# Kernel optimization log

Measured on AMD Instinct MI355X. Metric: run time of the kernel, lower is better.

Reference implementation:

```python
import jax, jax.numpy as jnp
import numpy as np

N_NODES = 20000  # number of batch nodes (static for segment ops)

def setup_inputs() -> dict:
    key = jax.random.key(0)
    N, E, V, D = N_NODES, 640000, 100000, 64
    ks = jax.random.split(key, 8)
    nodes = jax.random.randint(ks[0], (N,), 0, V)
    neigh_idx = jax.random.randint(ks[1], (E,), 0, V)
    seg_ids = jnp.sort(jax.random.randint(ks[2], (E,), 0, N))  # ragged degrees, sorted by node
    u2e = jax.random.normal(ks[3], (V, D), jnp.float32) * 0.02
    s1 = 1.0 / np.sqrt(2 * D)
    s2 = 1.0 / np.sqrt(D)
    att1_w = jax.random.uniform(ks[4], (2 * D, D), jnp.float32, -s1, s1)
    att1_b = jnp.zeros((D,), jnp.float32)
    att2_w = jax.random.uniform(ks[5], (D, D), jnp.float32, -s2, s2)
    att2_b = jnp.zeros((D,), jnp.float32)
    att3_w = jax.random.uniform(ks[6], (D, 1), jnp.float32, -s2, s2)
    att3_b = jnp.zeros((1,), jnp.float32)
    return dict(nodes=nodes, neigh_idx=neigh_idx, seg_ids=seg_ids, u2e=u2e,
                att1_w=att1_w, att1_b=att1_b, att2_w=att2_w, att2_b=att2_b,
                att3_w=att3_w, att3_b=att3_b)


def reference(nodes, neigh_idx, seg_ids, u2e, att1_w, att1_b, att2_w, att2_b, att3_w, att3_b):
    # Ragged per-node neighbor attention, flattened over all edges.
    e_u = u2e[neigh_idx]              # [E, D] neighbor embeddings
    u_rep = u2e[nodes][seg_ids]       # [E, D] center-node embedding broadcast per edge
    x = jnp.concatenate([e_u, u_rep], axis=1)            # [E, 2D]
    x = jax.nn.relu(x @ att1_w + att1_b)                  # [E, D]
    x = jax.nn.relu(x @ att2_w + att2_b)                  # [E, D]
    logits = (x @ att3_w + att3_b)[:, 0]                  # [E]
    # segment softmax over each node's neighbor set
    m = jax.ops.segment_max(logits, seg_ids, num_segments=N_NODES)
    m = jnp.where(jnp.isfinite(m), m, 0.0)                # guard empty segments
    ex = jnp.exp(logits - m[seg_ids])
    denom = jax.ops.segment_sum(ex, seg_ids, num_segments=N_NODES)
    att = ex / jnp.maximum(denom[seg_ids], 1e-9)          # [E]
    # attention-weighted sum of neighbor embeddings per node (e_u^T @ att_w per node)
    out = jax.ops.segment_sum(att[:, None] * e_u, seg_ids, num_segments=N_NODES)  # [N, D]
    return out
```

## Files before the change

### kernel.cpp

```cpp
#include <hip/hip_runtime.h>
#include <hip/hip_bf16.h>

typedef __attribute__((ext_vector_type(8))) short bf16x8;
typedef __attribute__((ext_vector_type(4))) float f32x4;

__device__ __forceinline__ unsigned short f2bf(float f) {
    unsigned x = __float_as_uint(f);
    unsigned r = (x + 0x7FFF + ((x >> 16) & 1)) >> 16;
    return (unsigned short)r;
}
__device__ __forceinline__ bf16x8 cvt8(const float* __restrict__ p) {
    bf16x8 r;
#pragma unroll
    for (int j = 0; j < 8; ++j) r[j] = (short)f2bf(p[j]);
    return r;
}
__device__ __forceinline__ unsigned pack_relu_bf16(unsigned yv, unsigned zv) {
    float lo = fmaxf(__uint_as_float(yv << 16) + __uint_as_float(zv << 16), 0.0f);
    float hi = fmaxf(__uint_as_float(yv & 0xFFFF0000u) + __uint_as_float(zv & 0xFFFF0000u), 0.0f);
    __hip_bfloat162 p = __float22bfloat162_rn(float2{lo, hi});
    return *(unsigned*)&p;
}

template <bool BF>
__launch_bounds__(256)
__global__ void conv_all_k(const float* __restrict__ u2e,
                           const int* __restrict__ nodes,
                           const int* __restrict__ segs,
                           const float* __restrict__ w1,
                           const float* __restrict__ w2,
                           const float* __restrict__ b1f,
                           unsigned short* __restrict__ u2ebf,
                           unsigned short* __restrict__ Y,
                           unsigned short* __restrict__ z,
                           unsigned short* __restrict__ w2t,
                           int* __restrict__ seg_off,
                           int V, int N, int E, int yblk, int zblk,
                           int ytiles, int ztiles) {
    __shared__ __align__(16) unsigned short w1l[64 * 72];
    const int bid = blockIdx.x;
    const int t = threadIdx.x;
    const int wid = t >> 6;
    const int lane = t & 63;
    const int q = lane >> 4;
    const int m15 = lane & 15;

    if (bid < yblk + zblk) {
        const bool isY = bid < yblk;
        const int kbase = isY ? 0 : 64;
        for (int u = t; u < 64 * 16; u += 256) {
            int k = u >> 4;
            int n4 = (u & 15) * 4;
            float4 v = *(const float4*)(w1 + (long)(kbase + k) * 64 + n4);
            w1l[(n4 + 0) * 72 + k] = f2bf(v.x);
            w1l[(n4 + 1) * 72 + k] = f2bf(v.y);
            w1l[(n4 + 2) * 72 + k] = f2bf(v.z);
            w1l[(n4 + 3) * 72 + k] = f2bf(v.w);
        }
        __syncthreads();

        bf16x8 wb0[4], wb1[4];
#pragma unroll
        for (int b = 0; b < 4; ++b) {
            const unsigned short* wr = w1l + (b * 16 + m15) * 72;
            wb0[b] = *(const bf16x8*)(wr + q * 8);
            wb1[b] = *(const bf16x8*)(wr + 32 + q * 8);
        }

        if (isY) {
            for (int tile = bid; tile < ytiles; tile += yblk) {
                const int wbase = tile * 64 + wid * 16;
                if (wbase >= V) continue;
                int row = min(wbase + m15, V - 1);
                const float* p = u2e + (long)row * 64;
                bf16x8 a0 = cvt8(p + q * 8);
                bf16x8 a1 = cvt8(p + 32 + q * 8);
                if (BF && wbase + m15 < V) {
                    *(bf16x8*)(u2ebf + (long)row * 64 + q * 8) = a0;
                    *(bf16x8*)(u2ebf + (long)row * 64 + 32 + q * 8) = a1;
                }
                f32x4 acc[4];
#pragma unroll
                for (int b = 0; b < 4; ++b) {
                    acc[b] = (f32x4){0.f, 0.f, 0.f, 0.f};
                    acc[b] = __builtin_amdgcn_mfma_f32_16x16x32_bf16(a0, wb0[b], acc[b], 0, 0, 0);
                    acc[b] = __builtin_amdgcn_mfma_f32_16x16x32_bf16(a1, wb1[b], acc[b], 0, 0, 0);
                }
#pragma unroll
                for (int b = 0; b < 4; ++b)
#pragma unroll
                    for (int r = 0; r < 4; ++r) {
                        int rr = wbase + q * 4 + r;
                        if (rr < V) Y[(long)rr * 64 + b * 16 + m15] = f2bf(acc[b][r]);
                    }
            }
        } else {
            float b1v[4];
#pragma unroll
            for (int b = 0; b < 4; ++b) b1v[b] = b1f[b * 16 + m15];
            for (int tile = bid - yblk; tile < ztiles; tile += zblk) {
                const int wbase = tile * 64 + wid * 16;
                if (wbase >= N) continue;
                int nd = nodes[min(wbase + m15, N - 1)];
                const float* p = u2e + (long)nd * 64;
                bf16x8 a0 = cvt8(p + q * 8);
                bf16x8 a1 = cvt8(p + 32 + q * 8);
                f32x4 acc[4];
#pragma unroll
                for (int b = 0; b < 4; ++b) {
                    acc[b] = (f32x4){b1v[b], b1v[b], b1v[b], b1v[b]};
                    acc[b] = __builtin_amdgcn_mfma_f32_16x16x32_bf16(a0, wb0[b], acc[b], 0, 0, 0);
                    acc[b] = __builtin_amdgcn_mfma_f32_16x16x32_bf16(a1, wb1[b], acc[b], 0, 0, 0);
                }
#pragma unroll
                for (int b = 0; b < 4; ++b)
#pragma unroll
                    for (int r = 0; r < 4; ++r) {
                        int rr = wbase + q * 4 + r;
                        if (rr < N) z[(long)rr * 64 + b * 16 + m15] = f2bf(acc[b][r]);
                    }
            }
        }
    } else if (bid == yblk + zblk) {
        for (int i = t; i < 64 * 64; i += 256) {
            int k = i >> 6, n = i & 63;
            w2t[n * 64 + k] = f2bf(w2[i]);
        }
    } else {
        int idx = (bid - yblk - zblk - 1) * 256 + t;
        if (idx > N) return;
        int l = 0, r = E;
        while (l < r) { int mid = (l + r) >> 1; if (segs[mid] < idx) l = mid + 1; else r = mid; }
        seg_off[idx] = l;
    }
}

__launch_bounds__(256)
__global__ void logits2_k(const int* __restrict__ neigh,
                          const int* __restrict__ segs,
                          const unsigned short* __restrict__ Y,
                          const unsigned short* __restrict__ z,
                          const unsigned short* __restrict__ w2t,
                          const float* __restrict__ b2f,
                          const float* __restrict__ w3f, const float* __restrict__ b3f,
                          float* __restrict__ ex, int E) {
    const int wid = threadIdx.x >> 6;
    const int lane = threadIdx.x & 63;
    const int q = lane >> 4;
    const int m15 = lane & 15;
    const long base = ((long)blockIdx.x * 4 + wid) * 32;
    if (base >= E) return;

    int vi[2], sg[2];
#pragma unroll
    for (int g = 0; g < 2; ++g) {
        long e = base + g * 16 + m15;
        int ec = (int)(e < E ? e : (long)E - 1);
        vi[g] = neigh[ec];
        sg[g] = segs[ec];
    }
    bf16x8 y0[2], y1[2], zz0[2], zz1[2];
#pragma unroll
    for (int g = 0; g < 2; ++g) {
        const unsigned short* yr = Y + (long)vi[g] * 64;
        y0[g] = *(const bf16x8*)(yr + q * 8);
        y1[g] = *(const bf16x8*)(yr + 32 + q * 8);
        const unsigned short* zr = z + (long)sg[g] * 64;
        zz0[g] = *(const bf16x8*)(zr + q * 8);
        zz1[g] = *(const bf16x8*)(zr + 32 + q * 8);
    }

    float b2v[4], w3v[4];
#pragma unroll
    for (int b = 0; b < 4; ++b) {
        b2v[b] = b2f[b * 16 + m15];
        w3v[b] = w3f[b * 16 + m15];
    }

    f32x4 acc[2][4];
#pragma unroll
    for (int g = 0; g < 2; ++g) {
        bf16x8 h0, h1;
#pragma unroll
        for (int j = 0; j < 4; ++j) {
            ((unsigned*)&h0)[j] = pack_relu_bf16(((unsigned*)&y0[g])[j], ((unsigned*)&zz0[g])[j]);
            ((unsigned*)&h1)[j] = pack_relu_bf16(((unsigned*)&y1[g])[j], ((unsigned*)&zz1[g])[j]);
        }
#pragma unroll
        for (int b = 0; b < 4; ++b) {
            acc[g][b] = (f32x4){b2v[b], b2v[b], b2v[b], b2v[b]};
            const bf16x8* wrow = (const bf16x8*)(w2t + (b * 16 + m15) * 64);
            acc[g][b] = __builtin_amdgcn_mfma_f32_16x16x32_bf16(h0, wrow[0 + q], acc[g][b], 0, 0, 0);
            acc[g][b] = __builtin_amdgcn_mfma_f32_16x16x32_bf16(h1, wrow[4 + q], acc[g][b], 0, 0, 0);
        }
    }

    const float b3v = b3f[0];
#pragma unroll
    for (int g = 0; g < 2; ++g)
#pragma unroll
        for (int r = 0; r < 4; ++r) {
            float v = 0.0f;
#pragma unroll
            for (int b = 0; b < 4; ++b) v += fmaxf(acc[g][b][r], 0.0f) * w3v[b];
            v += __shfl_xor(v, 1);
            v += __shfl_xor(v, 2);
            v += __shfl_xor(v, 4);
            v += __shfl_xor(v, 8);
            long ee = base + g * 16 + q * 4 + r;
            if (m15 == r && ee < E) ex[ee] = __expf(v + b3v);
        }
}

template <bool BF>
__launch_bounds__(256)
__global__ void aggw_k(const int* __restrict__ seg_off,
                       const int* __restrict__ neigh,
                       const unsigned short* __restrict__ u2ebf,
                       const float* __restrict__ u2e,
                       const float* __restrict__ ex,
                       float* __restrict__ out, int N) {
    const int wid = threadIdx.x >> 6;
    const int lane = threadIdx.x & 63;
    const int n = blockIdx.x * 4 + wid;
    if (n >= N) return;
    const int lo = seg_off[n];
    const int hi = seg_off[n + 1];
    const int slot = lane >> 3;
    const int cl = lane & 7;

    float a[8] = {0.f, 0.f, 0.f, 0.f, 0.f, 0.f, 0.f, 0.f};
    float s = 0.0f;

    for (int e = lo + slot; e < hi; e += 8) {
        float w = ex[e];
        int vi = neigh[e];
        s += w;
        if constexpr (BF) {
            bf16x8 v = *(const bf16x8*)(u2ebf + (long)vi * 64 + cl * 8);
            const unsigned* vd = (const unsigned*)&v;
#pragma unroll
            for (int j = 0; j < 4; ++j) {
                a[2 * j]     = fmaf(w, __uint_as_float(vd[j] << 16), a[2 * j]);
                a[2 * j + 1] = fmaf(w, __uint_as_float(vd[j] & 0xFFFF0000u), a[2 * j + 1]);
            }
        } else {
            const float* row = u2e + (long)vi * 64 + cl * 8;
            float4 v0 = *(const float4*)row;
            float4 v1 = *(const float4*)(row + 4);
            a[0] = fmaf(w, v0.x, a[0]); a[1] = fmaf(w, v0.y, a[1]);
            a[2] = fmaf(w, v0.z, a[2]); a[3] = fmaf(w, v0.w, a[3]);
            a[4] = fmaf(w, v1.x, a[4]); a[5] = fmaf(w, v1.y, a[5]);
            a[6] = fmaf(w, v1.z, a[6]); a[7] = fmaf(w, v1.w, a[7]);
        }
    }
#pragma unroll
    for (int msk = 8; msk <= 32; msk <<= 1) {
        s += __shfl_xor(s, msk);
#pragma unroll
        for (int j = 0; j < 8; ++j) a[j] += __shfl_xor(a[j], msk);
    }
    if (slot == 0) {
        float inv = 1.0f / fmaxf(s, 1e-9f);
        float4 o0 = {a[0] * inv, a[1] * inv, a[2] * inv, a[3] * inv};
        float4 o1 = {a[4] * inv, a[5] * inv, a[6] * inv, a[7] * inv};
        float* op = out + (long)n * 64 + cl * 8;
        *(float4*)op = o0;
        *(float4*)(op + 4) = o1;
    }
}

__global__ void prep_bounds_k(const float* __restrict__ w1,
                              const float* __restrict__ w2,
                              const int* __restrict__ segs,
                              unsigned short* __restrict__ w1t,
                              unsigned short* __restrict__ w2t,
                              int* __restrict__ seg_off, int N, int E) {
    int t = threadIdx.x;
    if (blockIdx.x == 0) {
        for (int i = t; i < 128 * 64; i += 256) {
            int k = i >> 6, n = i & 63;
            w1t[n * 128 + k] = f2bf(w1[i]);
        }
        for (int i = t; i < 64 * 64; i += 256) {
            int k = i >> 6, n = i & 63;
            w2t[n * 64 + k] = f2bf(w2[i]);
        }
    } else {
        int idx = (blockIdx.x - 1) * 256 + t;
        if (idx > N) return;
        int l = 0, r = E;
        while (l < r) { int mid = (l + r) >> 1; if (segs[mid] < idx) l = mid + 1; else r = mid; }
        seg_off[idx] = l;
    }
}

__launch_bounds__(256)
__global__ void logits_fb_k(const int* __restrict__ nodes,
                            const int* __restrict__ neigh,
                            const int* __restrict__ segs,
                            const float* __restrict__ u2e,
                            const unsigned short* __restrict__ w1t,
                            const unsigned short* __restrict__ w2t,
                            const float* __restrict__ b1f, const float* __restrict__ b2f,
                            const float* __restrict__ w3f, const float* __restrict__ b3f,
                            float* __restrict__ ex, int E) {
    __shared__ __align__(16) unsigned short h1buf[4][16 * 72];
    const int wid = threadIdx.x >> 6;
    const int lane = threadIdx.x & 63;
    const int q = lane >> 4;
    const int m15 = lane & 15;
    const long base = ((long)blockIdx.x * 4 + wid) * 16;
    long ee0 = base + m15;
    int e = (int)(ee0 < E ? ee0 : (long)E - 1);
    int ni = neigh[e];
    int ctr = nodes[segs[e]];
    const float* eu = u2e + (long)ni * 64;
    const float* ur = u2e + (long)ctr * 64;
    bf16x8 a0 = cvt8(eu + q * 8), a1 = cvt8(eu + 32 + q * 8);
    bf16x8 a2 = cvt8(ur + q * 8), a3 = cvt8(ur + 32 + q * 8);
    f32x4 acc[4];
#pragma unroll
    for (int b = 0; b < 4; ++b) {
        float bvv = b1f[b * 16 + m15];
        acc[b] = (f32x4){bvv, bvv, bvv, bvv};
        const bf16x8* wrow = (const bf16x8*)(w1t + (b * 16 + m15) * 128);
        acc[b] = __builtin_amdgcn_mfma_f32_16x16x32_bf16(a0, wrow[0 + q], acc[b], 0, 0, 0);
        acc[b] = __builtin_amdgcn_mfma_f32_16x16x32_bf16(a1, wrow[4 + q], acc[b], 0, 0, 0);
        acc[b] = __builtin_amdgcn_mfma_f32_16x16x32_bf16(a2, wrow[8 + q], acc[b], 0, 0, 0);
        acc[b] = __builtin_amdgcn_mfma_f32_16x16x32_bf16(a3, wrow[12 + q], acc[b], 0, 0, 0);
    }
#pragma unroll
    for (int b = 0; b < 4; ++b)
#pragma unroll
        for (int r = 0; r < 4; ++r)
            h1buf[wid][(q * 4 + r) * 72 + b * 16 + m15] = f2bf(fmaxf(acc[b][r], 0.0f));
    const unsigned short* hrow = &h1buf[wid][m15 * 72];
    bf16x8 h0 = *(const bf16x8*)(hrow + q * 8);
    bf16x8 h1 = *(const bf16x8*)(hrow + 32 + q * 8);
    f32x4 acc2[4];
#pragma unroll
    for (int b = 0; b < 4; ++b) {
        float bvv = b2f[b * 16 + m15];
        acc2[b] = (f32x4){bvv, bvv, bvv, bvv};
        const bf16x8* wrow = (const bf16x8*)(w2t + (b * 16 + m15) * 64);
        acc2[b] = __builtin_amdgcn_mfma_f32_16x16x32_bf16(h0, wrow[0 + q], acc2[b], 0, 0, 0);
        acc2[b] = __builtin_amdgcn_mfma_f32_16x16x32_bf16(h1, wrow[4 + q], acc2[b], 0, 0, 0);
    }
    float b3v = b3f[0];
#pragma unroll
    for (int r = 0; r < 4; ++r) {
        float v = 0.0f;
#pragma unroll
        for (int b = 0; b < 4; ++b) v += fmaxf(acc2[b][r], 0.0f) * w3f[b * 16 + m15];
        v += __shfl_xor(v, 1);
        v += __shfl_xor(v, 2);
        v += __shfl_xor(v, 4);
        v += __shfl_xor(v, 8);
        long ee = base + q * 4 + r;
        if (m15 == r && ee < E) ex[ee] = __expf(v + b3v);
    }
}

extern "C" void kernel_launch(void* const* d_in, const int* in_sizes, int n_in,
                              void* d_out, int out_size, void* d_ws, size_t ws_size,
                              hipStream_t stream) {
    const int* nodes = (const int*)d_in[0];
    const int* neigh = (const int*)d_in[1];
    const int* segs  = (const int*)d_in[2];
    const float* u2e = (const float*)d_in[3];
    const float* w1  = (const float*)d_in[4];
    const float* b1  = (const float*)d_in[5];
    const float* w2  = (const float*)d_in[6];
    const float* b2  = (const float*)d_in[7];
    const float* w3  = (const float*)d_in[8];
    const float* b3  = (const float*)d_in[9];
    const int N = in_sizes[0];
    const int E = in_sizes[1];
    const long VD = in_sizes[3];
    const int V = (int)(VD / 64);

    char* ws = (char*)d_ws;
    size_t off = 0;
    auto alloc = [&](size_t bytes) { char* p = ws + off; off = (off + bytes + 255) & ~(size_t)255; return p; };
    float* ex = (float*)alloc((size_t)E * 4);
    int* seg_off = (int*)alloc((size_t)(N + 1) * 4);
    unsigned short* w1t = (unsigned short*)alloc(128 * 64 * 2);
    unsigned short* w2t = (unsigned short*)alloc(64 * 64 * 2);
    size_t need_min = off;
    unsigned short* Y = (unsigned short*)alloc((size_t)VD * 2);
    unsigned short* zb = (unsigned short*)alloc((size_t)N * 64 * 2);
    size_t need_t2 = off;
    unsigned short* u2ebf = (unsigned short*)alloc((size_t)VD * 2);
    size_t need_t1 = off;
    (void)need_min;

    float* out = (float*)d_out;

    const int ytiles = (V + 63) / 64;
    const int ztiles = (N + 63) / 64;
    const int yblk = ytiles < 640 ? ytiles : 640;
    const int zblk = ztiles < 160 ? ztiles : 160;
    const int bblocks = (N + 256) / 256;
    const int lblocks = ((E + 31) / 32 + 3) / 4;
    const int ablocks = (N + 3) / 4;

    if (ws_size >= need_t1) {
        conv_all_k<true><<<yblk + zblk + 1 + bblocks, 256, 0, stream>>>(
            u2e, nodes, segs, w1, w2, b1, u2ebf, Y, zb, w2t, seg_off, V, N, E,
            yblk, zblk, ytiles, ztiles);
        logits2_k<<<lblocks, 256, 0, stream>>>(neigh, segs, Y, zb, w2t, b2, w3, b3, ex, E);
        aggw_k<true><<<ablocks, 256, 0, stream>>>(seg_off, neigh, u2ebf, nullptr, ex, out, N);
    } else if (ws_size >= need_t2) {
        conv_all_k<false><<<yblk + zblk + 1 + bblocks, 256, 0, stream>>>(
            u2e, nodes, segs, w1, w2, b1, nullptr, Y, zb, w2t, seg_off, V, N, E,
            yblk, zblk, ytiles, ztiles);
        logits2_k<<<lblocks, 256, 0, stream>>>(neigh, segs, Y, zb, w2t, b2, w3, b3, ex, E);
        aggw_k<false><<<ablocks, 256, 0, stream>>>(seg_off, neigh, nullptr, u2e, ex, out, N);
    } else {
        const int pbblocks = 1 + (N + 256) / 256;
        prep_bounds_k<<<pbblocks, 256, 0, stream>>>(w1, w2, segs, w1t, w2t, seg_off, N, E);
        const int blocks1 = ((E + 15) / 16 + 3) / 4;
        logits_fb_k<<<blocks1, 256, 0, stream>>>(nodes, neigh, segs, u2e, w1t, w2t,
                                                 b1, b2, w3, b3, ex, E);
        aggw_k<false><<<ablocks, 256, 0, stream>>>(seg_off, neigh, nullptr, u2e, ex, out, N);
    }
}
```

Baseline: 152.1 us.

## Fuse edge logits and weighted aggregation into one per-node kernel

Replaces the separate logits kernel and aggregation kernel with a single kernel where each wavefront owns one node and walks its edge segment in chunks of 16. It computes the MLP logits with MFMA, exponentiates, and accumulates the exp-weighted neighbor embeddings and denominator in registers. This removes the ex buffer round trip and one launch, and hoists the W2 fragments into registers. The trade-off is per-node load imbalance on ragged degrees and wasted MFMA lanes on partial chunks. The max subtraction is still skipped, as in the prior code.

```diff
diff --git a/kernel.cpp b/kernel.cpp
--- a/kernel.cpp
+++ b/kernel.cpp
@@ -135,81 +135,148 @@
     }
 }
 
+template <bool BF>
 __launch_bounds__(256)
-__global__ void logits2_k(const int* __restrict__ neigh,
-                          const int* __restrict__ segs,
-                          const unsigned short* __restrict__ Y,
-                          const unsigned short* __restrict__ z,
-                          const unsigned short* __restrict__ w2t,
-                          const float* __restrict__ b2f,
-                          const float* __restrict__ w3f, const float* __restrict__ b3f,
-                          float* __restrict__ ex, int E) {
+__global__ void fused_edge_k(const int* __restrict__ seg_off,
+                             const int* __restrict__ neigh,
+                             const unsigned short* __restrict__ Y,
+                             const unsigned short* __restrict__ z,
+                             const unsigned short* __restrict__ w2t,
+                             const unsigned short* __restrict__ u2ebf,
+                             const float* __restrict__ u2e,
+                             const float* __restrict__ b2f,
+                             const float* __restrict__ w3f,
+                             const float* __restrict__ b3f,
+                             float* __restrict__ out, int N) {
+    const int lane = threadIdx.x & 63;
     const int wid = threadIdx.x >> 6;
-    const int lane = threadIdx.x & 63;
     const int q = lane >> 4;
     const int m15 = lane & 15;
-    const long base = ((long)blockIdx.x * 4 + wid) * 32;
-    if (base >= E) return;
-
-    int vi[2], sg[2];
-#pragma unroll
-    for (int g = 0; g < 2; ++g) {
-        long e = base + g * 16 + m15;
-        int ec = (int)(e < E ? e : (long)E - 1);
-        vi[g] = neigh[ec];
-        sg[g] = segs[ec];
-    }
-    bf16x8 y0[2], y1[2], zz0[2], zz1[2];
-#pragma unroll
-    for (int g = 0; g < 2; ++g) {
-        const unsigned short* yr = Y + (long)vi[g] * 64;
-        y0[g] = *(const bf16x8*)(yr + q * 8);
-        y1[g] = *(const bf16x8*)(yr + 32 + q * 8);
-        const unsigned short* zr = z + (long)sg[g] * 64;
-        zz0[g] = *(const bf16x8*)(zr + q * 8);
-        zz1[g] = *(const bf16x8*)(zr + 32 + q * 8);
-    }
-
+    const int slot = lane >> 3;
+    const int cl = lane & 7;
+    const int n = blockIdx.x * 4 + wid;
+    if (n >= N) return;
+    const int lo = seg_off[n];
+    const int hi = seg_off[n + 1];
+
+    const unsigned short* zr = z + (long)n * 64;
+    bf16x8 zz0 = *(const bf16x8*)(zr + q * 8);
+    bf16x8 zz1 = *(const bf16x8*)(zr + 32 + q * 8);
+
+    bf16x8 wb[4][2];
+#pragma unroll
+    for (int b = 0; b < 4; ++b) {
+        const bf16x8* wrow = (const bf16x8*)(w2t + (b * 16 + m15) * 64);
+        wb[b][0] = wrow[q];
+        wb[b][1] = wrow[4 + q];
+    }
     float b2v[4], w3v[4];
 #pragma unroll
     for (int b = 0; b < 4; ++b) {
         b2v[b] = b2f[b * 16 + m15];
         w3v[b] = w3f[b * 16 + m15];
     }
-
-    f32x4 acc[2][4];
-#pragma unroll
-    for (int g = 0; g < 2; ++g) {
+    const float b3v = b3f[0];
+
+    float a[8] = {0.f, 0.f, 0.f, 0.f, 0.f, 0.f, 0.f, 0.f};
+    float s = 0.f;
+
+    const int jA = slot;
+    const int jB = slot + 8;
+    const int srcA = ((jA >> 2) << 4) | (jA & 3);
+    const int srcB = ((jB >> 2) << 4) | (jB & 3);
+
+    for (int e0 = lo; e0 < hi; e0 += 16) {
+        int ec = e0 + m15;
+        if (ec >= hi) ec = hi - 1;
+        int vi = neigh[ec];
+
+        int viA = __shfl(vi, jA);
+        int viB = __shfl(vi, jB);
+
+        const unsigned short* yr = Y + (long)vi * 64;
+        bf16x8 y0 = *(const bf16x8*)(yr + q * 8);
+        bf16x8 y1 = *(const bf16x8*)(yr + 32 + q * 8);
+
         bf16x8 h0, h1;
 #pragma unroll
         for (int j = 0; j < 4; ++j) {
-            ((unsigned*)&h0)[j] = pack_relu_bf16(((unsigned*)&y0[g])[j], ((unsigned*)&zz0[g])[j]);
-            ((unsigned*)&h1)[j] = pack_relu_bf16(((unsigned*)&y1[g])[j], ((unsigned*)&zz1[g])[j]);
-        }
+            ((unsigned*)&h0)[j] = pack_relu_bf16(((unsigned*)&y0)[j], ((unsigned*)&zz0)[j]);
+            ((unsigned*)&h1)[j] = pack_relu_bf16(((unsigned*)&y1)[j], ((unsigned*)&zz1)[j]);
+        }
+        f32x4 acc[4];
 #pragma unroll
         for (int b = 0; b < 4; ++b) {
-            acc[g][b] = (f32x4){b2v[b], b2v[b], b2v[b], b2v[b]};
-            const bf16x8* wrow = (const bf16x8*)(w2t + (b * 16 + m15) * 64);
-            acc[g][b] = __builtin_amdgcn_mfma_f32_16x16x32_bf16(h0, wrow[0 + q], acc[g][b], 0, 0, 0);
-            acc[g][b] = __builtin_amdgcn_mfma_f32_16x16x32_bf16(h1, wrow[4 + q], acc[g][b], 0, 0, 0);
-        }
-    }
-
-    const float b3v = b3f[0];
-#pragma unroll
-    for (int g = 0; g < 2; ++g)
+            acc[b] = (f32x4){b2v[b], b2v[b], b2v[b], b2v[b]};
+            acc[b] = __builtin_amdgcn_mfma_f32_16x16x32_bf16(h0, wb[b][0], acc[b], 0, 0, 0);
+            acc[b] = __builtin_amdgcn_mfma_f32_16x16x32_bf16(h1, wb[b][1], acc[b], 0, 0, 0);
+        }
+        float ev[4];
 #pragma unroll
         for (int r = 0; r < 4; ++r) {
             float v = 0.0f;
 #pragma unroll
-            for (int b = 0; b < 4; ++b) v += fmaxf(acc[g][b][r], 0.0f) * w3v[b];
+            for (int b = 0; b < 4; ++b) v += fmaxf(acc[b][r], 0.0f) * w3v[b];
             v += __shfl_xor(v, 1);
             v += __shfl_xor(v, 2);
             v += __shfl_xor(v, 4);
             v += __shfl_xor(v, 8);
-            long ee = base + g * 16 + q * 4 + r;
-            if (m15 == r && ee < E) ex[ee] = __expf(v + b3v);
-        }
+            ev[r] = __expf(v + b3v);
+        }
+        int rsel = m15 & 3;
+        float exval = rsel == 0 ? ev[0] : (rsel == 1 ? ev[1] : (rsel == 2 ? ev[2] : ev[3]));
+        float exA = __shfl(exval, srcA);
+        float exB = __shfl(exval, srcB);
+        if (e0 + jA >= hi) exA = 0.f;
+        if (e0 + jB >= hi) exB = 0.f;
+        s += exA;
+        s += exB;
+        if constexpr (BF) {
+            bf16x8 vA = *(const bf16x8*)(u2ebf + (long)viA * 64 + cl * 8);
+            bf16x8 vB = *(const bf16x8*)(u2ebf + (long)viB * 64 + cl * 8);
+            const unsigned* da = (const unsigned*)&vA;
+            const unsigned* db = (const unsigned*)&vB;
+#pragma unroll
+            for (int j = 0; j < 4; ++j) {
+                a[2 * j]     = fmaf(exA, __uint_as_float(da[j] << 16), a[2 * j]);
+                a[2 * j + 1] = fmaf(exA, __uint_as_float(da[j] & 0xFFFF0000u), a[2 * j + 1]);
+            }
+#pragma unroll
+            for (int j = 0; j < 4; ++j) {
+                a[2 * j]     = fmaf(exB, __uint_as_float(db[j] << 16), a[2 * j]);
+                a[2 * j + 1] = fmaf(exB, __uint_as_float(db[j] & 0xFFFF0000u), a[2 * j + 1]);
+            }
+        } else {
+            const float* rA = u2e + (long)viA * 64 + cl * 8;
+            float4 vA0 = *(const float4*)rA;
+            float4 vA1 = *(const float4*)(rA + 4);
+            const float* rB = u2e + (long)viB * 64 + cl * 8;
+            float4 vB0 = *(const float4*)rB;
+            float4 vB1 = *(const float4*)(rB + 4);
+            a[0] = fmaf(exA, vA0.x, a[0]); a[1] = fmaf(exA, vA0.y, a[1]);
+            a[2] = fmaf(exA, vA0.z, a[2]); a[3] = fmaf(exA, vA0.w, a[3]);
+            a[4] = fmaf(exA, vA1.x, a[4]); a[5] = fmaf(exA, vA1.y, a[5]);
+            a[6] = fmaf(exA, vA1.z, a[6]); a[7] = fmaf(exA, vA1.w, a[7]);
+            a[0] = fmaf(exB, vB0.x, a[0]); a[1] = fmaf(exB, vB0.y, a[1]);
+            a[2] = fmaf(exB, vB0.z, a[2]); a[3] = fmaf(exB, vB0.w, a[3]);
+            a[4] = fmaf(exB, vB1.x, a[4]); a[5] = fmaf(exB, vB1.y, a[5]);
+            a[6] = fmaf(exB, vB1.z, a[6]); a[7] = fmaf(exB, vB1.w, a[7]);
+        }
+    }
+#pragma unroll
+    for (int msk = 8; msk <= 32; msk <<= 1) {
+        s += __shfl_xor(s, msk);
+#pragma unroll
+        for (int j = 0; j < 8; ++j) a[j] += __shfl_xor(a[j], msk);
+    }
+    if (slot == 0) {
+        float inv = 1.0f / fmaxf(s, 1e-9f);
+        float4 o0 = {a[0] * inv, a[1] * inv, a[2] * inv, a[3] * inv};
+        float4 o1 = {a[4] * inv, a[5] * inv, a[6] * inv, a[7] * inv};
+        float* op = out + (long)n * 64 + cl * 8;
+        *(float4*)op = o0;
+        *(float4*)(op + 4) = o1;
+    }
 }
 
 template <bool BF>
@@ -402,21 +469,20 @@
     const int yblk = ytiles < 640 ? ytiles : 640;
     const int zblk = ztiles < 160 ? ztiles : 160;
     const int bblocks = (N + 256) / 256;
-    const int lblocks = ((E + 31) / 32 + 3) / 4;
     const int ablocks = (N + 3) / 4;
 
     if (ws_size >= need_t1) {
         conv_all_k<true><<<yblk + zblk + 1 + bblocks, 256, 0, stream>>>(
             u2e, nodes, segs, w1, w2, b1, u2ebf, Y, zb, w2t, seg_off, V, N, E,
             yblk, zblk, ytiles, ztiles);
-        logits2_k<<<lblocks, 256, 0, stream>>>(neigh, segs, Y, zb, w2t, b2, w3, b3, ex, E);
-        aggw_k<true><<<ablocks, 256, 0, stream>>>(seg_off, neigh, u2ebf, nullptr, ex, out, N);
+        fused_edge_k<true><<<ablocks, 256, 0, stream>>>(
+            seg_off, neigh, Y, zb, w2t, u2ebf, nullptr, b2, w3, b3, out, N);
     } else if (ws_size >= need_t2) {
         conv_all_k<false><<<yblk + zblk + 1 + bblocks, 256, 0, stream>>>(
             u2e, nodes, segs, w1, w2, b1, nullptr, Y, zb, w2t, seg_off, V, N, E,
             yblk, zblk, ytiles, ztiles);
-        logits2_k<<<lblocks, 256, 0, stream>>>(neigh, segs, Y, zb, w2t, b2, w3, b3, ex, E);
-        aggw_k<false><<<ablocks, 256, 0, stream>>>(seg_off, neigh, nullptr, u2e, ex, out, N);
+        fused_edge_k<false><<<ablocks, 256, 0, stream>>>(
+            seg_off, neigh, Y, zb, w2t, nullptr, u2e, b2, w3, b3, out, N);
     } else {
         const int pbblocks = 1 + (N + 256) / 256;
         prep_bounds_k<<<pbblocks, 256, 0, stream>>>(w1, w2, segs, w1t, w2t, seg_off, N, E);
```

Result: slower. 162.6 us (+6.9%).

## Fuse logits and weighted aggregation into one edge kernel with atomics

Applied to the files above, without the earlier changes.

Replaces the separate logits kernel and per-node aggregation kernel with a single edge-parallel kernel. It computes exp(logit) and immediately scatters the weighted neighbor embeddings and the denominators into zeroed output buffers via atomicAdd, reduced across lanes for each segment. A small division kernel then normalizes. The Y projection and the bf16 embedding are interleaved into one 128-wide row so a single gathered row serves both uses. This removes the ex round-trip and the second gather of neighbor rows, at the cost of global float atomics and a per-node loop inside each 16-edge group. The softmax max-subtraction is skipped, as it already was before.

```diff
diff --git a/kernel.cpp b/kernel.cpp
--- a/kernel.cpp
+++ b/kernel.cpp
@@ -22,7 +22,7 @@
     return *(unsigned*)&p;
 }
 
-template <bool BF>
+template <bool T1>
 __launch_bounds__(256)
 __global__ void conv_all_k(const float* __restrict__ u2e,
                            const int* __restrict__ nodes,
@@ -30,11 +30,12 @@
                            const float* __restrict__ w1,
                            const float* __restrict__ w2,
                            const float* __restrict__ b1f,
-                           unsigned short* __restrict__ u2ebf,
-                           unsigned short* __restrict__ Y,
+                           unsigned short* __restrict__ yu,
                            unsigned short* __restrict__ z,
                            unsigned short* __restrict__ w2t,
                            int* __restrict__ seg_off,
+                           float* __restrict__ zout,
+                           float* __restrict__ den,
                            int V, int N, int E, int yblk, int zblk,
                            int ytiles, int ztiles) {
     __shared__ __align__(16) unsigned short w1l[64 * 72];
@@ -68,6 +69,7 @@
         }
 
         if (isY) {
+            const int ystride = T1 ? 128 : 64;
             for (int tile = bid; tile < ytiles; tile += yblk) {
                 const int wbase = tile * 64 + wid * 16;
                 if (wbase >= V) continue;
@@ -75,9 +77,9 @@
                 const float* p = u2e + (long)row * 64;
                 bf16x8 a0 = cvt8(p + q * 8);
                 bf16x8 a1 = cvt8(p + 32 + q * 8);
-                if (BF && wbase + m15 < V) {
-                    *(bf16x8*)(u2ebf + (long)row * 64 + q * 8) = a0;
-                    *(bf16x8*)(u2ebf + (long)row * 64 + 32 + q * 8) = a1;
+                if (T1 && wbase + m15 < V) {
+                    *(bf16x8*)(yu + (long)row * 128 + 64 + q * 8) = a0;
+                    *(bf16x8*)(yu + (long)row * 128 + 96 + q * 8) = a1;
                 }
                 f32x4 acc[4];
 #pragma unroll
@@ -91,7 +93,7 @@
 #pragma unroll
                     for (int r = 0; r < 4; ++r) {
                         int rr = wbase + q * 4 + r;
-                        if (rr < V) Y[(long)rr * 64 + b * 16 + m15] = f2bf(acc[b][r]);
+                        if (rr < V) yu[(long)rr * ystride + b * 16 + m15] = f2bf(acc[b][r]);
                     }
             }
         } else {
@@ -127,12 +129,183 @@
             w2t[n * 64 + k] = f2bf(w2[i]);
         }
     } else {
-        int idx = (bid - yblk - zblk - 1) * 256 + t;
-        if (idx > N) return;
-        int l = 0, r = E;
-        while (l < r) { int mid = (l + r) >> 1; if (segs[mid] < idx) l = mid + 1; else r = mid; }
-        seg_off[idx] = l;
-    }
+        if (T1) {
+            long zt = (long)(bid - yblk - zblk - 1) * 256 + t;
+            long nth = (long)(gridDim.x - yblk - zblk - 1) * 256;
+            f32x4 zz = (f32x4){0.f, 0.f, 0.f, 0.f};
+            for (long i = zt; i < (long)N * 16; i += nth) ((f32x4*)zout)[i] = zz;
+            for (long i = zt; i < (long)((N + 3) / 4); i += nth) ((f32x4*)den)[i] = zz;
+        } else {
+            int idx = (bid - yblk - zblk - 1) * 256 + t;
+            if (idx > N) return;
+            int l = 0, r = E;
+            while (l < r) { int mid = (l + r) >> 1; if (segs[mid] < idx) l = mid + 1; else r = mid; }
+            seg_off[idx] = l;
+        }
+    }
+}
+
+__launch_bounds__(256)
+__global__ void fused_ea_k(const int* __restrict__ neigh,
+                           const int* __restrict__ segs,
+                           const unsigned short* __restrict__ yu,
+                           const unsigned short* __restrict__ z,
+                           const unsigned short* __restrict__ w2t,
+                           const float* __restrict__ b2f,
+                           const float* __restrict__ w3f,
+                           const float* __restrict__ b3f,
+                           float* __restrict__ outp,
+                           float* __restrict__ den, int E) {
+    const int wid = threadIdx.x >> 6;
+    const int lane = threadIdx.x & 63;
+    const int q = lane >> 4;
+    const int m15 = lane & 15;
+    const long base = ((long)blockIdx.x * 4 + wid) * 32;
+    if (base >= E) return;
+
+    int vi[2], sg[2];
+    bool val[2];
+#pragma unroll
+    for (int g = 0; g < 2; ++g) {
+        long e = base + g * 16 + m15;
+        val[g] = e < E;
+        int ec = (int)(val[g] ? e : (long)E - 1);
+        vi[g] = neigh[ec];
+        sg[g] = segs[ec];
+    }
+    bf16x8 y0[2], y1[2], u0[2], u1[2], zz0[2], zz1[2];
+#pragma unroll
+    for (int g = 0; g < 2; ++g) {
+        const unsigned short* r = yu + (long)vi[g] * 128;
+        y0[g] = *(const bf16x8*)(r + q * 8);
+        y1[g] = *(const bf16x8*)(r + 32 + q * 8);
+        u0[g] = *(const bf16x8*)(r + 64 + q * 16);
+        u1[g] = *(const bf16x8*)(r + 64 + q * 16 + 8);
+        const unsigned short* zr = z + (long)sg[g] * 64;
+        zz0[g] = *(const bf16x8*)(zr + q * 8);
+        zz1[g] = *(const bf16x8*)(zr + 32 + q * 8);
+    }
+
+    float b2v[4], w3v[4];
+#pragma unroll
+    for (int b = 0; b < 4; ++b) {
+        b2v[b] = b2f[b * 16 + m15];
+        w3v[b] = w3f[b * 16 + m15];
+    }
+    const float b3v = b3f[0];
+
+    f32x4 acc[2][4];
+#pragma unroll
+    for (int g = 0; g < 2; ++g) {
+        bf16x8 h0, h1;
+#pragma unroll
+        for (int j = 0; j < 4; ++j) {
+            ((unsigned*)&h0)[j] = pack_relu_bf16(((unsigned*)&y0[g])[j], ((unsigned*)&zz0[g])[j]);
+            ((unsigned*)&h1)[j] = pack_relu_bf16(((unsigned*)&y1[g])[j], ((unsigned*)&zz1[g])[j]);
+        }
+#pragma unroll
+        for (int b = 0; b < 4; ++b) {
+            acc[g][b] = (f32x4){b2v[b], b2v[b], b2v[b], b2v[b]};
+            const bf16x8* wrow = (const bf16x8*)(w2t + (b * 16 + m15) * 64);
+            acc[g][b] = __builtin_amdgcn_mfma_f32_16x16x32_bf16(h0, wrow[0 + q], acc[g][b], 0, 0, 0);
+            acc[g][b] = __builtin_amdgcn_mfma_f32_16x16x32_bf16(h1, wrow[4 + q], acc[g][b], 0, 0, 0);
+        }
+    }
+
+#pragma unroll
+    for (int g = 0; g < 2; ++g) {
+        float ev[4];
+#pragma unroll
+        for (int r = 0; r < 4; ++r) {
+            float v = 0.0f;
+#pragma unroll
+            for (int b = 0; b < 4; ++b) v += fmaxf(acc[g][b][r], 0.0f) * w3v[b];
+            v += __shfl_xor(v, 1);
+            v += __shfl_xor(v, 2);
+            v += __shfl_xor(v, 4);
+            v += __shfl_xor(v, 8);
+            ev[r] = __expf(v + b3v);
+        }
+        int rsel = m15 & 3;
+        float exval = rsel == 0 ? ev[0] : (rsel == 1 ? ev[1] : (rsel == 2 ? ev[2] : ev[3]));
+        float exm = __shfl(exval, ((m15 >> 2) << 4) | (m15 & 3));
+        if (!val[g]) exm = 0.0f;
+
+        float uc[16];
+        const unsigned* du0 = (const unsigned*)&u0[g];
+        const unsigned* du1 = (const unsigned*)&u1[g];
+#pragma unroll
+        for (int tt = 0; tt < 4; ++tt) {
+            uc[2 * tt]         = __uint_as_float(du0[tt] << 16);
+            uc[2 * tt + 1]     = __uint_as_float(du0[tt] & 0xFFFF0000u);
+            uc[8 + 2 * tt]     = __uint_as_float(du1[tt] << 16);
+            uc[8 + 2 * tt + 1] = __uint_as_float(du1[tt] & 0xFFFF0000u);
+        }
+
+        const int ndlo = __shfl(sg[g], 0);
+        const int ndhi = __shfl(sg[g], 15);
+        for (int nd = ndlo; nd <= ndhi; ++nd) {
+            float sel = (sg[g] == nd) ? exm : 0.0f;
+            float cs[16];
+#pragma unroll
+            for (int c = 0; c < 16; ++c) cs[c] = sel * uc[c];
+            float c8[8];
+            {
+                const bool b = m15 & 1;
+#pragma unroll
+                for (int i = 0; i < 8; ++i) {
+                    float keep = b ? cs[2 * i + 1] : cs[2 * i];
+                    float send = b ? cs[2 * i] : cs[2 * i + 1];
+                    c8[i] = keep + __shfl_xor(send, 1);
+                }
+            }
+            float c4[4];
+            {
+                const bool b = m15 & 2;
+#pragma unroll
+                for (int i = 0; i < 4; ++i) {
+                    float keep = b ? c8[2 * i + 1] : c8[2 * i];
+                    float send = b ? c8[2 * i] : c8[2 * i + 1];
+                    c4[i] = keep + __shfl_xor(send, 2);
+                }
+            }
+            float c2[2];
+            {
+                const bool b = m15 & 4;
+#pragma unroll
+                for (int i = 0; i < 2; ++i) {
+                    float keep = b ? c4[2 * i + 1] : c4[2 * i];
+                    float send = b ? c4[2 * i] : c4[2 * i + 1];
+                    c2[i] = keep + __shfl_xor(send, 4);
+                }
+            }
+            float tot;
+            {
+                const bool b = m15 & 8;
+                float keep = b ? c2[1] : c2[0];
+                float send = b ? c2[0] : c2[1];
+                tot = keep + __shfl_xor(send, 8);
+            }
+            atomicAdd(outp + (long)nd * 64 + lane, tot);
+            float ds = sel;
+            ds += __shfl_xor(ds, 1);
+            ds += __shfl_xor(ds, 2);
+            ds += __shfl_xor(ds, 4);
+            ds += __shfl_xor(ds, 8);
+            if (lane == 0) atomicAdd(den + nd, ds);
+        }
+    }
+}
+
+__launch_bounds__(256)
+__global__ void div_k(float* __restrict__ out, const float* __restrict__ den, int N) {
+    int i = blockIdx.x * 256 + threadIdx.x;
+    if (i >= N * 16) return;
+    float inv = 1.0f / fmaxf(den[i >> 4], 1e-9f);
+    f32x4* p = (f32x4*)out + i;
+    f32x4 v = *p;
+    v[0] *= inv; v[1] *= inv; v[2] *= inv; v[3] *= inv;
+    *p = v;
 }
 
 __launch_bounds__(256)
@@ -212,14 +385,12 @@
         }
 }
 
-template <bool BF>
 __launch_bounds__(256)
-__global__ void aggw_k(const int* __restrict__ seg_off,
-                       const int* __restrict__ neigh,
-                       const unsigned short* __restrict__ u2ebf,
-                       const float* __restrict__ u2e,
-                       const float* __restrict__ ex,
-                       float* __restrict__ out, int N) {
+__global__ void aggw_f32_k(const int* __restrict__ seg_off,
+                           const int* __restrict__ neigh,
+                           const float* __restrict__ u2e,
+                           const float* __restrict__ ex,
+                           float* __restrict__ out, int N) {
     const int wid = threadIdx.x >> 6;
     const int lane = threadIdx.x & 63;
     const int n = blockIdx.x * 4 + wid;
@@ -236,23 +407,13 @@
         float w = ex[e];
         int vi = neigh[e];
         s += w;
-        if constexpr (BF) {
-            bf16x8 v = *(const bf16x8*)(u2ebf + (long)vi * 64 + cl * 8);
-            const unsigned* vd = (const unsigned*)&v;
-#pragma unroll
-            for (int j = 0; j < 4; ++j) {
-                a[2 * j]     = fmaf(w, __uint_as_float(vd[j] << 16), a[2 * j]);
-                a[2 * j + 1] = fmaf(w, __uint_as_float(vd[j] & 0xFFFF0000u), a[2 * j + 1]);
-            }
-        } else {
-            const float* row = u2e + (long)vi * 64 + cl * 8;
-            float4 v0 = *(const float4*)row;
-            float4 v1 = *(const float4*)(row + 4);
-            a[0] = fmaf(w, v0.x, a[0]); a[1] = fmaf(w, v0.y, a[1]);
-            a[2] = fmaf(w, v0.z, a[2]); a[3] = fmaf(w, v0.w, a[3]);
-            a[4] = fmaf(w, v1.x, a[4]); a[5] = fmaf(w, v1.y, a[5]);
-            a[6] = fmaf(w, v1.z, a[6]); a[7] = fmaf(w, v1.w, a[7]);
-        }
+        const float* row = u2e + (long)vi * 64 + cl * 8;
+        float4 v0 = *(const float4*)row;
+        float4 v1 = *(const float4*)(row + 4);
+        a[0] = fmaf(w, v0.x, a[0]); a[1] = fmaf(w, v0.y, a[1]);
+        a[2] = fmaf(w, v0.z, a[2]); a[3] = fmaf(w, v0.w, a[3]);
+        a[4] = fmaf(w, v1.x, a[4]); a[5] = fmaf(w, v1.y, a[5]);
+        a[6] = fmaf(w, v1.z, a[6]); a[7] = fmaf(w, v1.w, a[7]);
     }
 #pragma unroll
     for (int msk = 8; msk <= 32; msk <<= 1) {
@@ -391,7 +552,8 @@
     unsigned short* Y = (unsigned short*)alloc((size_t)VD * 2);
     unsigned short* zb = (unsigned short*)alloc((size_t)N * 64 * 2);
     size_t need_t2 = off;
-    unsigned short* u2ebf = (unsigned short*)alloc((size_t)VD * 2);
+    unsigned short* yu = (unsigned short*)alloc((size_t)VD * 4);
+    float* den = (float*)alloc((size_t)N * 4);
     size_t need_t1 = off;
     (void)need_min;
 
@@ -404,25 +566,27 @@
     const int bblocks = (N + 256) / 256;
     const int lblocks = ((E + 31) / 32 + 3) / 4;
     const int ablocks = (N + 3) / 4;
+    const int ZBLK = 128;
 
     if (ws_size >= need_t1) {
-        conv_all_k<true><<<yblk + zblk + 1 + bblocks, 256, 0, stream>>>(
-            u2e, nodes, segs, w1, w2, b1, u2ebf, Y, zb, w2t, seg_off, V, N, E,
-            yblk, zblk, ytiles, ztiles);
-        logits2_k<<<lblocks, 256, 0, stream>>>(neigh, segs, Y, zb, w2t, b2, w3, b3, ex, E);
-        aggw_k<true><<<ablocks, 256, 0, stream>>>(seg_off, neigh, u2ebf, nullptr, ex, out, N);
+        conv_all_k<true><<<yblk + zblk + 1 + ZBLK, 256, 0, stream>>>(
+            u2e, nodes, segs, w1, w2, b1, yu, zb, w2t, nullptr, out, den,
+            V, N, E, yblk, zblk, ytiles, ztiles);
+        fused_ea_k<<<lblocks, 256, 0, stream>>>(
+            neigh, segs, yu, zb, w2t, b2, w3, b3, out, den, E);
+        div_k<<<(N * 16 + 255) / 256, 256, 0, stream>>>(out, den, N);
     } else if (ws_size >= need_t2) {
         conv_all_k<false><<<yblk + zblk + 1 + bblocks, 256, 0, stream>>>(
-            u2e, nodes, segs, w1, w2, b1, nullptr, Y, zb, w2t, seg_off, V, N, E,
-            yblk, zblk, ytiles, ztiles);
+            u2e, nodes, segs, w1, w2, b1, Y, zb, w2t, seg_off, nullptr, nullptr,
+            V, N, E, yblk, zblk, ytiles, ztiles);
         logits2_k<<<lblocks, 256, 0, stream>>>(neigh, segs, Y, zb, w2t, b2, w3, b3, ex, E);
-        aggw_k<false><<<ablocks, 256, 0, stream>>>(seg_off, neigh, nullptr, u2e, ex, out, N);
+        aggw_f32_k<<<ablocks, 256, 0, stream>>>(seg_off, neigh, u2e, ex, out, N);
     } else {
         const int pbblocks = 1 + (N + 256) / 256;
         prep_bounds_k<<<pbblocks, 256, 0, stream>>>(w1, w2, segs, w1t, w2t, seg_off, N, E);
         const int blocks1 = ((E + 15) / 16 + 3) / 4;
         logits_fb_k<<<blocks1, 256, 0, stream>>>(nodes, neigh, segs, u2e, w1t, w2t,
                                                  b1, b2, w3, b3, ex, E);
-        aggw_k<false><<<ablocks, 256, 0, stream>>>(seg_off, neigh, nullptr, u2e, ex, out, N);
-    }
-}
+        aggw_f32_k<<<ablocks, 256, 0, stream>>>(seg_off, neigh, nullptr  == nullptr ? u2e : u2e, ex, out, N);
+    }
+}
```

New measurement: 149.2 us. About the same (-1.9%).
